# Kernel tuning notes

Hardware: AMD Instinct MI355X
Metric: run time of the kernel (lower is better)

Reference implementation:

```python
import jax, jax.numpy as jnp
import numpy as np

N_HEADS = 6
HEAD_SIZE = 64


def setup_inputs() -> dict:
    key = jax.random.key(0)
    k1, k2, k3, k4 = jax.random.split(key, 4)
    B, T, C = 8, 2048, N_HEADS * HEAD_SIZE
    x = jax.random.normal(k1, (B, T, C), dtype=jnp.float32)
    # small init scale keeps softmax logits in a sane range
    w_qkv = jax.random.normal(k2, (C, 3 * C), dtype=jnp.float32) * 0.05
    w_proj = jax.random.normal(k3, (C, C), dtype=jnp.float32) * 0.05
    b_proj = jax.random.normal(k4, (C,), dtype=jnp.float32) * 0.05
    return {"x": x, "w_qkv": w_qkv, "w_proj": w_proj, "b_proj": b_proj}


def reference(x, w_qkv, w_proj, b_proj):
    B, T, C = x.shape
    qkv = x @ w_qkv                      # [B, T, 3C]
    q, k, v = jnp.split(qkv, 3, axis=2)
    # [B, T, C] -> [B, H, T, D]
    def heads(t):
        return t.reshape(B, T, N_HEADS, HEAD_SIZE).transpose(0, 2, 1, 3)
    q, k, v = heads(q), heads(k), heads(v)
    scale = HEAD_SIZE ** -0.5
    scores = jnp.einsum('bhqd,bhkd->bhqk', q, k) * scale   # [B, H, T, T]
    causal = jnp.tril(jnp.ones((T, T), dtype=bool))
    scores = jnp.where(causal[None, None], scores, jnp.float32(-jnp.inf))
    weights = jax.nn.softmax(scores, axis=-1)
    # dropout is identity in eval mode
    out = jnp.einsum('bhqk,bhkd->bhqd', weights, v)          # [B, H, T, D]
    out = out.transpose(0, 2, 1, 3).reshape(B, T, C)
    return out @ w_proj + b_proj
```

## Files before the change

kernel.cpp:

```cpp
#include <hip/hip_runtime.h>
#include <hip/hip_bf16.h>

typedef __bf16 bf16_t;
typedef __bf16 bf16x8 __attribute__((ext_vector_type(8)));
typedef __bf16 bf16x4 __attribute__((ext_vector_type(4)));
typedef float floatx4 __attribute__((ext_vector_type(4)));

#define MFMA16(a, b, c) __builtin_amdgcn_mfma_f32_16x16x32_bf16(a, b, c, 0, 0, 0)

#if __has_builtin(__builtin_amdgcn_exp2f)
#define EXP2F(x) __builtin_amdgcn_exp2f(x)
#else
#define EXP2F(x) __expf((x)*0.693147180559945f)
#endif

__device__ __forceinline__ void async_copy16(const bf16_t* g, bf16_t* l) {
    __builtin_amdgcn_global_load_lds((const __attribute__((address_space(1))) void*)g,
                                     (__attribute__((address_space(3))) void*)l, 16, 0, 0);
}

__global__ void prep_fused(const float* __restrict__ x, const float* __restrict__ w_qkv,
                           const float* __restrict__ w_proj, bf16_t* __restrict__ xb,
                           bf16_t* __restrict__ wqkvT, bf16_t* __restrict__ wprojT) {
    const int bx = blockIdx.x, tid = threadIdx.x;
    if (bx < 3072) {
        size_t i = ((size_t)bx * 256 + tid) * 8;
        float4 v0 = *(const float4*)(x + i);
        float4 v1 = *(const float4*)(x + i + 4);
        bf16x8 o = {(bf16_t)v0.x, (bf16_t)v0.y, (bf16_t)v0.z, (bf16_t)v0.w,
                    (bf16_t)v1.x, (bf16_t)v1.y, (bf16_t)v1.z, (bf16_t)v1.w};
        *(bf16x8*)(xb + i) = o;
        return;
    }
    __shared__ float tile[32][33];
    int which, n0, k0, Nd;
    if (bx < 3072 + 432) {
        int idx = bx - 3072;
        which = 0; Nd = 1152; n0 = (idx % 36) * 32; k0 = (idx / 36) * 32;
    } else {
        int idx = bx - 3072 - 432;
        which = 1; Nd = 384; n0 = (idx % 12) * 32; k0 = (idx / 12) * 32;
    }
    const float* in = which ? w_proj : w_qkv;
    bf16_t* out = which ? wprojT : wqkvT;
    const int tx = tid & 31, ty = tid >> 5;
#pragma unroll
    for (int i = 0; i < 4; i++)
        tile[ty + i * 8][tx] = in[(size_t)(k0 + ty + i * 8) * Nd + n0 + tx];
    __syncthreads();
#pragma unroll
    for (int i = 0; i < 4; i++) {
        int n = n0 + ty + i * 8;
        float v = tile[tx][ty + i * 8];
        if (!which && n < 384) v *= 0.1803368851f;
        out[(size_t)n * 384 + k0 + tx] = (bf16_t)v;
    }
}

__global__ __launch_bounds__(256, 3)
void gemm_qkv(const bf16_t* __restrict__ A, const bf16_t* __restrict__ Bt,
              bf16_t* __restrict__ qkv, bf16_t* __restrict__ Vt, int M, int N, int K) {
    __shared__ __align__(16) bf16_t As[2][128 * 32];
    __shared__ __align__(16) bf16_t Bs[2][128 * 32];
    const int tid = threadIdx.x;
    const int wave = tid >> 6, lane = tid & 63;
    const int wm = wave >> 1, wn = wave & 1;
    const int quad = lane >> 4, l16 = lane & 15;
    const int row0 = blockIdx.y * 128, col0 = blockIdx.x * 128;
    const int swz = l16 & 3;

    floatx4 acc[4][4];
#pragma unroll
    for (int i = 0; i < 4; i++)
#pragma unroll
        for (int j = 0; j < 4; j++) acc[i][j] = (floatx4){0.f, 0.f, 0.f, 0.f};

    auto stage = [&](int buf, int k0) {
#pragma unroll
        for (int it = 0; it < 2; it++) {
            int cb = wave * 64 + it * 256;
            int c = cb + lane;
            int r = c >> 2;
            int col = k0 + (((c & 3) ^ (r & 3)) * 8);
            async_copy16(A + (size_t)(row0 + r) * K + col, &As[buf][0] + cb * 8);
            async_copy16(Bt + (size_t)(col0 + r) * K + col, &Bs[buf][0] + cb * 8);
        }
    };

    const int nk = K >> 5;
    stage(0, 0);
    for (int kt = 0; kt < nk; kt++) {
        __syncthreads();
        if (kt + 1 < nk) stage((kt + 1) & 1, (kt + 1) * 32);
        const bf16_t* as = &As[kt & 1][0];
        const bf16_t* bs = &Bs[kt & 1][0];
        bf16x8 af[4], bfr[4];
#pragma unroll
        for (int i = 0; i < 4; i++)
            af[i] = *(const bf16x8*)(as + (wm * 64 + i * 16 + l16) * 32 + ((quad ^ swz) * 8));
#pragma unroll
        for (int j = 0; j < 4; j++)
            bfr[j] = *(const bf16x8*)(bs + (wn * 64 + j * 16 + l16) * 32 + ((quad ^ swz) * 8));
#pragma unroll
        for (int i = 0; i < 4; i++)
#pragma unroll
            for (int j = 0; j < 4; j++) acc[i][j] = MFMA16(bfr[j], af[i], acc[i][j]);
    }
    if (col0 < 768) {
#pragma unroll
        for (int i = 0; i < 4; i++) {
            const size_t row = (size_t)(row0 + wm * 64 + i * 16 + l16);
#pragma unroll
            for (int j = 0; j < 4; j++) {
                const int colb = col0 + wn * 64 + j * 16 + quad * 4;
                bf16x4 v = {(bf16_t)acc[i][j][0], (bf16_t)acc[i][j][1],
                            (bf16_t)acc[i][j][2], (bf16_t)acc[i][j][3]};
                *(bf16x4*)(qkv + row * N + colb) = v;
            }
        }
    } else {
        __syncthreads();
        bf16_t* myb = &As[0][0] + wave * 4096;
#pragma unroll
        for (int i = 0; i < 4; i++)
#pragma unroll
            for (int j = 0; j < 4; j++)
#pragma unroll
                for (int r = 0; r < 4; r++) {
                    int d2 = j * 16 + quad * 4 + r;
                    int t2 = i * 16 + l16;
                    myb[d2 * 64 + (((t2 >> 3) ^ (d2 & 7)) * 8) + (t2 & 7)] =
                        (bf16_t)acc[i][j][r];
                }
        asm volatile("s_waitcnt lgkmcnt(0)" ::: "memory");
        const int row_t = row0 + wm * 64;
        const int b = row_t >> 11;
        const int tt = (row_t & 2047) >> 6;
        const int h = (col0 - 768 + wn * 64) >> 6;
        bf16_t* vout = Vt + (((size_t)(b * 6 + h) * 32 + tt) << 12);
#pragma unroll
        for (int it = 0; it < 8; it++) {
            int d2 = it * 8 + (lane >> 3);
            int cl = lane & 7;
            bf16x8 v = *(const bf16x8*)(myb + d2 * 64 + ((cl ^ (d2 & 7)) * 8));
            *(bf16x8*)(vout + d2 * 64 + cl * 8) = v;
        }
    }
}

__global__ __launch_bounds__(256, 3)
void gemm_out(const bf16_t* __restrict__ A, const bf16_t* __restrict__ Bt,
              float* __restrict__ C, int M, int N, int K, const float* __restrict__ bias) {
    __shared__ __align__(16) bf16_t As[2][64 * 32];
    __shared__ __align__(16) bf16_t Bs[2][128 * 32];
    const int tid = threadIdx.x;
    const int wave = tid >> 6, lane = tid & 63;
    const int wm = wave >> 1, wn = wave & 1;
    const int quad = lane >> 4, l16 = lane & 15;
    const int row0 = blockIdx.y * 64, col0 = blockIdx.x * 128;
    const int swz = l16 & 3;

    floatx4 acc[2][4];
#pragma unroll
    for (int i = 0; i < 2; i++)
#pragma unroll
        for (int j = 0; j < 4; j++) acc[i][j] = (floatx4){0.f, 0.f, 0.f, 0.f};

    auto stage = [&](int buf, int k0) {
        {
            int c = wave * 64 + lane;
            int r = c >> 2;
            int col = k0 + (((c & 3) ^ (r & 3)) * 8);
            async_copy16(A + (size_t)(row0 + r) * K + col, &As[buf][0] + (wave * 64) * 8);
        }
#pragma unroll
        for (int it = 0; it < 2; it++) {
            int cb = wave * 64 + it * 256;
            int c = cb + lane;
            int r = c >> 2;
            int col = k0 + (((c & 3) ^ (r & 3)) * 8);
            async_copy16(Bt + (size_t)(col0 + r) * K + col, &Bs[buf][0] + cb * 8);
        }
    };

    const int nk = K >> 5;
    stage(0, 0);
    for (int kt = 0; kt < nk; kt++) {
        __syncthreads();
        if (kt + 1 < nk) stage((kt + 1) & 1, (kt + 1) * 32);
        const bf16_t* as = &As[kt & 1][0];
        const bf16_t* bs = &Bs[kt & 1][0];
        bf16x8 af[2], bfr[4];
#pragma unroll
        for (int i = 0; i < 2; i++)
            af[i] = *(const bf16x8*)(as + (wm * 32 + i * 16 + l16) * 32 + ((quad ^ swz) * 8));
#pragma unroll
        for (int j = 0; j < 4; j++)
            bfr[j] = *(const bf16x8*)(bs + (wn * 64 + j * 16 + l16) * 32 + ((quad ^ swz) * 8));
#pragma unroll
        for (int i = 0; i < 2; i++)
#pragma unroll
            for (int j = 0; j < 4; j++) acc[i][j] = MFMA16(bfr[j], af[i], acc[i][j]);
    }
#pragma unroll
    for (int i = 0; i < 2; i++) {
        const size_t row = (size_t)(row0 + wm * 32 + i * 16 + l16);
#pragma unroll
        for (int j = 0; j < 4; j++) {
            const int colb = col0 + wn * 64 + j * 16 + quad * 4;
            float4 bv = *(const float4*)(bias + colb);
            float4 v = {acc[i][j][0] + bv.x, acc[i][j][1] + bv.y,
                        acc[i][j][2] + bv.z, acc[i][j][3] + bv.w};
            *(float4*)(C + row * N + colb) = v;
        }
    }
}

__device__ __forceinline__ void stage64(const bf16_t* __restrict__ gtile, int stride,
                                        bf16_t* lds, int wave, int lane) {
#pragma unroll
    for (int it = 0; it < 2; it++) {
        int cb = wave * 64 + it * 256;
        int c = cb + lane;
        int r = c >> 3;
        int col = ((c & 7) ^ (r & 7)) * 8;
        async_copy16(gtile + (size_t)r * stride + col, lds + cb * 8);
    }
}

__global__ __launch_bounds__(256, 3)
void attn_kernel(const bf16_t* __restrict__ qkv, const bf16_t* __restrict__ Vt,
                 bf16_t* __restrict__ attn_out) {
    constexpr int T = 2048, C3 = 1152;
    const int bx = blockIdx.x, h = blockIdx.y, b = blockIdx.z;
    const int qa = bx, qb = 31 - bx;
    const int tid = threadIdx.x;
    const int wave = tid >> 6, lane = tid & 63;
    const int quad = lane >> 4, l16 = lane & 15;

    __shared__ __align__(16) bf16_t Ks[2][64 * 64];
    __shared__ __align__(16) bf16_t Vs[2][64 * 64];
    __shared__ __align__(16) bf16_t Ps[4][2][16 * 64];

    const bf16_t* kbase = qkv + (size_t)b * T * C3 + 384 + h * 64;
    const bf16_t* vbase = Vt + (((size_t)(b * 6 + h) * 32) << 12);

    const bf16_t* qpa =
        qkv + ((size_t)b * T + qa * 64 + wave * 16 + l16) * C3 + h * 64 + quad * 8;
    const bf16_t* qpb =
        qkv + ((size_t)b * T + qb * 64 + wave * 16 + l16) * C3 + h * 64 + quad * 8;
    bf16x8 qA0 = *(const bf16x8*)qpa, qA1 = *(const bf16x8*)(qpa + 32);
    bf16x8 qB0 = *(const bf16x8*)qpb, qB1 = *(const bf16x8*)(qpb + 32);

    floatx4 oA[4], oB[4];
    float lpA = 0.f, lpB = 0.f;
#pragma unroll
    for (int r = 0; r < 4; r++) {
        oA[r] = (floatx4){0.f, 0.f, 0.f, 0.f};
        oB[r] = (floatx4){0.f, 0.f, 0.f, 0.f};
    }
    const floatx4 C0 = {-13.f, -13.f, -13.f, -13.f};

    stage64(kbase, C3, &Ks[0][0], wave, lane);
    stage64(vbase, 64, &Vs[0][0], wave, lane);

    const int swz = l16 & 7;
    bf16_t* psA = &Ps[wave][0][0];
    bf16_t* psB = &Ps[wave][1][0];

    for (int kt = 0; kt <= qb; kt++) {
        __syncthreads();
        if (kt < qb) {
            stage64(kbase + (size_t)(kt + 1) * 64 * C3, C3, &Ks[(kt + 1) & 1][0], wave, lane);
            stage64(vbase + ((kt + 1) << 12), 64, &Vs[(kt + 1) & 1][0], wave, lane);
        }
        const bf16_t* kb = &Ks[kt & 1][0];
        const bf16_t* vb = &Vs[kt & 1][0];
        const bool doA = (kt <= qa);

        bf16x8 kf[4][2];
#pragma unroll
        for (int nt = 0; nt < 4; nt++)
#pragma unroll
            for (int hh = 0; hh < 2; hh++)
                kf[nt][hh] = *(const bf16x8*)(kb + (nt * 16 + l16) * 64 +
                                              (((hh * 4 + quad) ^ swz) * 8));

        floatx4 sA[4], sB[4];
#pragma unroll
        for (int nt = 0; nt < 4; nt++) {
            sB[nt] = MFMA16(kf[nt][0], qB0, C0);
            sB[nt] = MFMA16(kf[nt][1], qB1, sB[nt]);
        }
        if (doA) {
#pragma unroll
            for (int nt = 0; nt < 4; nt++) {
                sA[nt] = MFMA16(kf[nt][0], qA0, C0);
                sA[nt] = MFMA16(kf[nt][1], qA1, sA[nt]);
            }
        }
        if (kt == qb) {
#pragma unroll
            for (int nt = 0; nt < 4; nt++)
#pragma unroll
                for (int r = 0; r < 4; r++)
                    if (nt * 16 + quad * 4 + r > wave * 16 + l16) sB[nt][r] = -1e30f;
        }
        if (kt == qa) {
#pragma unroll
            for (int nt = 0; nt < 4; nt++)
#pragma unroll
                for (int r = 0; r < 4; r++)
                    if (nt * 16 + quad * 4 + r > wave * 16 + l16) sA[nt][r] = -1e30f;
        }

#pragma unroll
        for (int nt = 0; nt < 4; nt++) {
#pragma unroll
            for (int r = 0; r < 4; r++) {
                float p = EXP2F(sB[nt][r]);
                sB[nt][r] = p;
                lpB += p;
            }
            bf16x4 p4 = {(bf16_t)sB[nt][0], (bf16_t)sB[nt][1],
                         (bf16_t)sB[nt][2], (bf16_t)sB[nt][3]};
            *(bf16x4*)(psB + l16 * 64 + (((nt * 2 + (quad >> 1)) ^ swz) * 8) +
                       (quad & 1) * 4) = p4;
        }
        if (doA) {
#pragma unroll
            for (int nt = 0; nt < 4; nt++) {
#pragma unroll
                for (int r = 0; r < 4; r++) {
                    float p = EXP2F(sA[nt][r]);
                    sA[nt][r] = p;
                    lpA += p;
                }
                bf16x4 p4 = {(bf16_t)sA[nt][0], (bf16_t)sA[nt][1],
                             (bf16_t)sA[nt][2], (bf16_t)sA[nt][3]};
                *(bf16x4*)(psA + l16 * 64 + (((nt * 2 + (quad >> 1)) ^ swz) * 8) +
                           (quad & 1) * 4) = p4;
            }
        }

        bf16x8 vf[4][2];
#pragma unroll
        for (int nt = 0; nt < 4; nt++)
#pragma unroll
            for (int hh = 0; hh < 2; hh++)
                vf[nt][hh] = *(const bf16x8*)(vb + (nt * 16 + l16) * 64 +
                                              (((hh * 4 + quad) ^ swz) * 8));

        asm volatile("s_waitcnt lgkmcnt(0)" ::: "memory");

        bf16x8 pB0 = *(const bf16x8*)(psB + l16 * 64 + ((quad ^ swz) * 8));
        bf16x8 pB1 = *(const bf16x8*)(psB + l16 * 64 + (((4 + quad) ^ swz) * 8));
#pragma unroll
        for (int dt = 0; dt < 4; dt++) {
            oB[dt] = MFMA16(vf[dt][0], pB0, oB[dt]);
            oB[dt] = MFMA16(vf[dt][1], pB1, oB[dt]);
        }
        if (doA) {
            bf16x8 pA0 = *(const bf16x8*)(psA + l16 * 64 + ((quad ^ swz) * 8));
            bf16x8 pA1 = *(const bf16x8*)(psA + l16 * 64 + (((4 + quad) ^ swz) * 8));
#pragma unroll
            for (int dt = 0; dt < 4; dt++) {
                oA[dt] = MFMA16(vf[dt][0], pA0, oA[dt]);
                oA[dt] = MFMA16(vf[dt][1], pA1, oA[dt]);
            }
        }
    }

    lpA += __shfl_xor(lpA, 16); lpA += __shfl_xor(lpA, 32);
    lpB += __shfl_xor(lpB, 16); lpB += __shfl_xor(lpB, 32);
    const float invA = 1.0f / lpA, invB = 1.0f / lpB;
    const int tA = qa * 64 + wave * 16 + l16, tB = qb * 64 + wave * 16 + l16;
#pragma unroll
    for (int dt = 0; dt < 4; dt++) {
        bf16x4 va = {(bf16_t)(oA[dt][0] * invA), (bf16_t)(oA[dt][1] * invA),
                     (bf16_t)(oA[dt][2] * invA), (bf16_t)(oA[dt][3] * invA)};
        bf16x4 vb4 = {(bf16_t)(oB[dt][0] * invB), (bf16_t)(oB[dt][1] * invB),
                      (bf16_t)(oB[dt][2] * invB), (bf16_t)(oB[dt][3] * invB)};
        int col = h * 64 + dt * 16 + quad * 4;
        *(bf16x4*)(attn_out + ((size_t)b * T + tA) * 384 + col) = va;
        *(bf16x4*)(attn_out + ((size_t)b * T + tB) * 384 + col) = vb4;
    }
}

extern "C" void kernel_launch(void* const* d_in, const int* in_sizes, int n_in,
                              void* d_out, int out_size, void* d_ws, size_t ws_size,
                              hipStream_t stream) {
    const float* x      = (const float*)d_in[0];
    const float* w_qkv  = (const float*)d_in[1];
    const float* w_proj = (const float*)d_in[2];
    const float* b_proj = (const float*)d_in[3];
    float* out = (float*)d_out;

    bf16_t* ws = (bf16_t*)d_ws;
    bf16_t* wqkvT = ws;
    bf16_t* wprojT = wqkvT + 1152 * 384;
    bf16_t* xb = wprojT + 384 * 384;
    bf16_t* qkv = xb + (size_t)16384 * 384;
    bf16_t* Vt = qkv + (size_t)16384 * 1152;
    bf16_t* attn = Vt + (size_t)48 * 64 * 2048;

    hipLaunchKernelGGL(prep_fused, dim3(3072 + 432 + 144), dim3(256), 0, stream,
                       x, w_qkv, w_proj, xb, wqkvT, wprojT);
    hipLaunchKernelGGL(gemm_qkv, dim3(9, 128), dim3(256), 0, stream,
                       xb, wqkvT, qkv, Vt, 16384, 1152, 384);
    hipLaunchKernelGGL(attn_kernel, dim3(16, 6, 8), dim3(256), 0, stream, qkv, Vt, attn);
    hipLaunchKernelGGL(gemm_out, dim3(3, 256), dim3(256), 0, stream,
                       attn, wprojT, out, 16384, 384, 384, b_proj);
}
```

Before: 179.4 us.

## Keep P in registers via permlane swaps, remap blocks per XCD, add setprio

The attention kernel no longer round-trips the softmax probabilities through LDS. It converts them with v_cvt_pk_bf16 and reshuffles them into the MFMA operand layout using permlane32/16 swaps, which removes the LDS writes, the wait and the reads. s_setprio is raised around the MFMA sections so waves in their matmul phase are favoured. All three main kernels switch to a 1D grid with a remapping that spreads consecutive block IDs across the 8 XCDs, which is meant to keep related tiles in the same L2. The risk is that the permlane layout must exactly match the old LDS transpose, and the remapping assumes the grid sizes divide evenly by 8.

```diff
diff --git a/kernel.cpp b/kernel.cpp
--- a/kernel.cpp
+++ b/kernel.cpp
@@ -5,6 +5,7 @@
 typedef __bf16 bf16x8 __attribute__((ext_vector_type(8)));
 typedef __bf16 bf16x4 __attribute__((ext_vector_type(4)));
 typedef float floatx4 __attribute__((ext_vector_type(4)));
+typedef unsigned uint32x2 __attribute__((ext_vector_type(2)));
 
 #define MFMA16(a, b, c) __builtin_amdgcn_mfma_f32_16x16x32_bf16(a, b, c, 0, 0, 0)
 
@@ -17,6 +18,43 @@
 __device__ __forceinline__ void async_copy16(const bf16_t* g, bf16_t* l) {
     __builtin_amdgcn_global_load_lds((const __attribute__((address_space(1))) void*)g,
                                      (__attribute__((address_space(3))) void*)l, 16, 0, 0);
+}
+
+__device__ __forceinline__ unsigned cvt_pk_bf16(float lo, float hi) {
+    unsigned r;
+    asm("v_cvt_pk_bf16_f32 %0, %1, %2" : "=v"(r) : "v"(lo), "v"(hi));
+    return r;
+}
+
+__device__ __forceinline__ void plane32(unsigned& x, unsigned& y) {
+#if __has_builtin(__builtin_amdgcn_permlane32_swap)
+    uint32x2 r = __builtin_amdgcn_permlane32_swap(x, y, false, false);
+    x = r[0]; y = r[1];
+#else
+    asm("v_permlane32_swap_b32 %0, %1" : "+v"(x), "+v"(y));
+#endif
+}
+__device__ __forceinline__ void plane16(unsigned& x, unsigned& y) {
+#if __has_builtin(__builtin_amdgcn_permlane16_swap)
+    uint32x2 r = __builtin_amdgcn_permlane16_swap(x, y, false, false);
+    x = r[0]; y = r[1];
+#else
+    asm("v_permlane16_swap_b32 %0, %1" : "+v"(x), "+v"(y));
+#endif
+}
+
+__device__ __forceinline__ bf16x8 pack_pfrag(const floatx4& sE, const floatx4& sO) {
+    unsigned a0 = cvt_pk_bf16(sE[0], sE[1]);
+    unsigned a1 = cvt_pk_bf16(sE[2], sE[3]);
+    unsigned b0 = cvt_pk_bf16(sO[0], sO[1]);
+    unsigned b1 = cvt_pk_bf16(sO[2], sO[3]);
+    plane32(a0, b0);
+    plane32(a1, b1);
+    plane16(a0, b0);
+    plane16(a1, b1);
+    union { unsigned u[4]; bf16x8 v; } r;
+    r.u[0] = a0; r.u[1] = a1; r.u[2] = b0; r.u[3] = b1;
+    return r.v;
 }
 
 __global__ void prep_fused(const float* __restrict__ x, const float* __restrict__ w_qkv,
@@ -62,11 +100,13 @@
               bf16_t* __restrict__ qkv, bf16_t* __restrict__ Vt, int M, int N, int K) {
     __shared__ __align__(16) bf16_t As[2][128 * 32];
     __shared__ __align__(16) bf16_t Bs[2][128 * 32];
+    const int nblk = blockIdx.x;
+    const int wgl = ((nblk & 7) * 144) + (nblk >> 3);
+    const int row0 = (wgl / 9) * 128, col0 = (wgl % 9) * 128;
     const int tid = threadIdx.x;
     const int wave = tid >> 6, lane = tid & 63;
     const int wm = wave >> 1, wn = wave & 1;
     const int quad = lane >> 4, l16 = lane & 15;
-    const int row0 = blockIdx.y * 128, col0 = blockIdx.x * 128;
     const int swz = l16 & 3;
 
     floatx4 acc[4][4];
@@ -153,11 +193,13 @@
               float* __restrict__ C, int M, int N, int K, const float* __restrict__ bias) {
     __shared__ __align__(16) bf16_t As[2][64 * 32];
     __shared__ __align__(16) bf16_t Bs[2][128 * 32];
+    const int nblk = blockIdx.x;
+    const int wgl = ((nblk & 7) * 96) + (nblk >> 3);
+    const int row0 = (wgl / 3) * 64, col0 = (wgl % 3) * 128;
     const int tid = threadIdx.x;
     const int wave = tid >> 6, lane = tid & 63;
     const int wm = wave >> 1, wn = wave & 1;
     const int quad = lane >> 4, l16 = lane & 15;
-    const int row0 = blockIdx.y * 64, col0 = blockIdx.x * 128;
     const int swz = l16 & 3;
 
     floatx4 acc[2][4];
@@ -232,7 +274,11 @@
 void attn_kernel(const bf16_t* __restrict__ qkv, const bf16_t* __restrict__ Vt,
                  bf16_t* __restrict__ attn_out) {
     constexpr int T = 2048, C3 = 1152;
-    const int bx = blockIdx.x, h = blockIdx.y, b = blockIdx.z;
+    const int nblk = blockIdx.x;
+    const int wgl = ((nblk & 7) * 96) + (nblk >> 3);
+    const int bx = wgl & 15;
+    const int g = wgl >> 4;
+    const int h = g % 6, b = g / 6;
     const int qa = bx, qb = 31 - bx;
     const int tid = threadIdx.x;
     const int wave = tid >> 6, lane = tid & 63;
@@ -240,7 +286,6 @@
 
     __shared__ __align__(16) bf16_t Ks[2][64 * 64];
     __shared__ __align__(16) bf16_t Vs[2][64 * 64];
-    __shared__ __align__(16) bf16_t Ps[4][2][16 * 64];
 
     const bf16_t* kbase = qkv + (size_t)b * T * C3 + 384 + h * 64;
     const bf16_t* vbase = Vt + (((size_t)(b * 6 + h) * 32) << 12);
@@ -265,8 +310,6 @@
     stage64(vbase, 64, &Vs[0][0], wave, lane);
 
     const int swz = l16 & 7;
-    bf16_t* psA = &Ps[wave][0][0];
-    bf16_t* psB = &Ps[wave][1][0];
 
     for (int kt = 0; kt <= qb; kt++) {
         __syncthreads();
@@ -287,6 +330,7 @@
                                               (((hh * 4 + quad) ^ swz) * 8));
 
         floatx4 sA[4], sB[4];
+        __builtin_amdgcn_s_setprio(1);
 #pragma unroll
         for (int nt = 0; nt < 4; nt++) {
             sB[nt] = MFMA16(kf[nt][0], qB0, C0);
@@ -299,6 +343,16 @@
                 sA[nt] = MFMA16(kf[nt][1], qA1, sA[nt]);
             }
         }
+        __builtin_amdgcn_s_setprio(0);
+
+        bf16x8 vf[4][2];
+#pragma unroll
+        for (int nt = 0; nt < 4; nt++)
+#pragma unroll
+            for (int hh = 0; hh < 2; hh++)
+                vf[nt][hh] = *(const bf16x8*)(vb + (nt * 16 + l16) * 64 +
+                                              (((hh * 4 + quad) ^ swz) * 8));
+
         if (kt == qb) {
 #pragma unroll
             for (int nt = 0; nt < 4; nt++)
@@ -315,60 +369,44 @@
         }
 
 #pragma unroll
-        for (int nt = 0; nt < 4; nt++) {
+        for (int nt = 0; nt < 4; nt++)
 #pragma unroll
             for (int r = 0; r < 4; r++) {
                 float p = EXP2F(sB[nt][r]);
                 sB[nt][r] = p;
                 lpB += p;
             }
-            bf16x4 p4 = {(bf16_t)sB[nt][0], (bf16_t)sB[nt][1],
-                         (bf16_t)sB[nt][2], (bf16_t)sB[nt][3]};
-            *(bf16x4*)(psB + l16 * 64 + (((nt * 2 + (quad >> 1)) ^ swz) * 8) +
-                       (quad & 1) * 4) = p4;
-        }
+        bf16x8 pB0 = pack_pfrag(sB[0], sB[1]);
+        bf16x8 pB1 = pack_pfrag(sB[2], sB[3]);
+
+        bf16x8 pA0, pA1;
         if (doA) {
 #pragma unroll
-            for (int nt = 0; nt < 4; nt++) {
+            for (int nt = 0; nt < 4; nt++)
 #pragma unroll
                 for (int r = 0; r < 4; r++) {
                     float p = EXP2F(sA[nt][r]);
                     sA[nt][r] = p;
                     lpA += p;
                 }
-                bf16x4 p4 = {(bf16_t)sA[nt][0], (bf16_t)sA[nt][1],
-                             (bf16_t)sA[nt][2], (bf16_t)sA[nt][3]};
-                *(bf16x4*)(psA + l16 * 64 + (((nt * 2 + (quad >> 1)) ^ swz) * 8) +
-                           (quad & 1) * 4) = p4;
-            }
-        }
-
-        bf16x8 vf[4][2];
-#pragma unroll
-        for (int nt = 0; nt < 4; nt++)
-#pragma unroll
-            for (int hh = 0; hh < 2; hh++)
-                vf[nt][hh] = *(const bf16x8*)(vb + (nt * 16 + l16) * 64 +
-                                              (((hh * 4 + quad) ^ swz) * 8));
-
-        asm volatile("s_waitcnt lgkmcnt(0)" ::: "memory");
-
-        bf16x8 pB0 = *(const bf16x8*)(psB + l16 * 64 + ((quad ^ swz) * 8));
-        bf16x8 pB1 = *(const bf16x8*)(psB + l16 * 64 + (((4 + quad) ^ swz) * 8));
+            pA0 = pack_pfrag(sA[0], sA[1]);
+            pA1 = pack_pfrag(sA[2], sA[3]);
+        }
+
+        __builtin_amdgcn_s_setprio(1);
 #pragma unroll
         for (int dt = 0; dt < 4; dt++) {
             oB[dt] = MFMA16(vf[dt][0], pB0, oB[dt]);
             oB[dt] = MFMA16(vf[dt][1], pB1, oB[dt]);
         }
         if (doA) {
-            bf16x8 pA0 = *(const bf16x8*)(psA + l16 * 64 + ((quad ^ swz) * 8));
-            bf16x8 pA1 = *(const bf16x8*)(psA + l16 * 64 + (((4 + quad) ^ swz) * 8));
 #pragma unroll
             for (int dt = 0; dt < 4; dt++) {
                 oA[dt] = MFMA16(vf[dt][0], pA0, oA[dt]);
                 oA[dt] = MFMA16(vf[dt][1], pA1, oA[dt]);
             }
         }
+        __builtin_amdgcn_s_setprio(0);
     }
 
     lpA += __shfl_xor(lpA, 16); lpA += __shfl_xor(lpA, 32);
@@ -406,9 +444,9 @@
 
     hipLaunchKernelGGL(prep_fused, dim3(3072 + 432 + 144), dim3(256), 0, stream,
                        x, w_qkv, w_proj, xb, wqkvT, wprojT);
-    hipLaunchKernelGGL(gemm_qkv, dim3(9, 128), dim3(256), 0, stream,
+    hipLaunchKernelGGL(gemm_qkv, dim3(1152), dim3(256), 0, stream,
                        xb, wqkvT, qkv, Vt, 16384, 1152, 384);
-    hipLaunchKernelGGL(attn_kernel, dim3(16, 6, 8), dim3(256), 0, stream, qkv, Vt, attn);
-    hipLaunchKernelGGL(gemm_out, dim3(3, 256), dim3(256), 0, stream,
+    hipLaunchKernelGGL(attn_kernel, dim3(768), dim3(256), 0, stream, qkv, Vt, attn);
+    hipLaunchKernelGGL(gemm_out, dim3(768), dim3(256), 0, stream,
                        attn, wprojT, out, 16384, 384, 384, b_proj);
 }
```

Result: faster. 169.4 us (median of 2 runs) (-5.6%).
